# Kernel tuning notes

Measured on AMD Instinct MI355X. Metric: run time of the kernel, lower is better.

The kernel has to match this reference:

```python
import jax, jax.numpy as jnp
import numpy as np

N, E, G = 50000, 800000, 512          # nodes, edges, graphs in batch
DIN, DH, H, DOUT = 128, 128, 2, 128   # dim_in, dim_h, heads, dim_out
NEG_SLOPE = 0.2
EPS_BN = 1e-5


def setup_inputs():
    key = jax.random.key(0)
    ks = jax.random.split(key, 12)
    def glorot(k, shape, fan):
        return (jax.random.normal(k, shape, jnp.float32) / np.float32(np.sqrt(fan)))
    return dict(
        x=jax.random.normal(ks[0], (N, DIN), jnp.float32),
        edge_index=jax.random.randint(ks[1], (2, E), 0, N, dtype=jnp.int32),
        batch=jnp.sort(jax.random.randint(ks[2], (N,), 0, G, dtype=jnp.int32)),
        Wl1=glorot(ks[3], (DIN, H * DH), DIN),
        Wr1=glorot(ks[4], (DIN, H * DH), DIN),
        att1=glorot(ks[5], (H, DH), DH),
        b1=jnp.zeros((H * DH,), jnp.float32),
        gamma=jnp.ones((H * DH,), jnp.float32),
        beta=jnp.zeros((H * DH,), jnp.float32),
        Wl2=glorot(ks[6], (H * DH, DOUT), H * DH),
        Wr2=glorot(ks[7], (H * DH, DOUT), H * DH),
        att2=glorot(ks[8], (1, DOUT), DOUT),
        b2=jnp.zeros((DOUT,), jnp.float32),
        Wlin=glorot(ks[9], (DOUT, 2), DOUT),
        blin=jnp.zeros((2,), jnp.float32),
    )


def gatv2_conv(x, src, dst, Wl, Wr, att, bias, heads, dh, n):
    # x: [n, F]; src/dst: [Etot] (self-loops already appended)
    xl = (x @ Wl).reshape(n, heads, dh)  # source transform (messages)
    xr = (x @ Wr).reshape(n, heads, dh)  # target transform
    m = xl[src] + xr[dst]                             # [Etot, H, dh]
    e = jnp.einsum('ehd,hd->eh', jax.nn.leaky_relu(m, NEG_SLOPE), att)  # [Etot, H]
    # softmax over incoming edges of each target node
    emax = jax.ops.segment_max(e, dst, num_segments=n)
    ex = jnp.exp(e - emax[dst])
    denom = jax.ops.segment_sum(ex, dst, num_segments=n)
    alpha = ex / (denom[dst] + 1e-16)                 # [Etot, H]
    out = jax.ops.segment_sum(xl[src] * alpha[:, :, None], dst, num_segments=n)
    return out.reshape(n, heads * dh) + bias


def reference(x, edge_index, batch, Wl1, Wr1, att1, b1, gamma, beta,
              Wl2, Wr2, att2, b2, Wlin, blin):
    loops = jnp.arange(N, dtype=edge_index.dtype)
    src = jnp.concatenate([edge_index[0], loops])
    dst = jnp.concatenate([edge_index[1], loops])

    h = gatv2_conv(x, src, dst, Wl1, Wr1, att1, b1, H, DH, N)   # [N, H*DH]
    h = jax.nn.elu(h)
    # BatchNorm over node dimension (training-mode batch stats)
    mu = h.mean(axis=0)
    var = h.var(axis=0)
    h = (h - mu) * jax.lax.rsqrt(var + EPS_BN) * gamma + beta
    # dropout p=0 -> identity
    h = gatv2_conv(h, src, dst, Wl2, Wr2, att2, b2, 1, DOUT, N)  # [N, DOUT]

    # global mean pool per graph
    s = jax.ops.segment_sum(h, batch, num_segments=G)
    cnt = jax.ops.segment_sum(jnp.ones((N,), h.dtype), batch, num_segments=G)
    pooled = s / jnp.maximum(cnt, 1.0)[:, None]                  # [G, DOUT]
    return pooled @ Wlin + blin                                  # [G, 2]
```

## Files before the change

kernel.cpp:

```cpp
#include <hip/hip_runtime.h>


#define DIN 128
#define F1 256
#define F2 128
#define NEG_SLOPE 0.2f

typedef unsigned short u16;
typedef __attribute__((ext_vector_type(8))) short short8;
typedef __attribute__((ext_vector_type(4))) float floatx4;

__device__ __forceinline__ float bf2f(u16 u) {
  return __uint_as_float(((unsigned int)u) << 16);
}
__device__ __forceinline__ u16 f2bf(float f) {
  unsigned int x = __float_as_uint(f);
  return (u16)((x + 0x7fffu + ((x >> 16) & 1u)) >> 16);
}
__device__ __forceinline__ void load8(const u16* p, float (&f)[8]) {
  short8 v = *(const short8*)p;
#pragma unroll
  for (int k = 0; k < 8; k++) f[k] = bf2f((u16)v[k]);
}

struct PTab { const void* src[8]; int off[9]; };
__global__ __launch_bounds__(256) void k_convert_all(
    const void* __restrict__ xsrc, u16* __restrict__ xb, int n4, int nxb,
    PTab t, u16* __restrict__ pb, int ptotal, int npb,
    const void* __restrict__ Wl1s, const void* __restrict__ Wr1s,
    const void* __restrict__ Wl2s, const void* __restrict__ Wr2s,
    u16* __restrict__ Wl1t, u16* __restrict__ Wr1t,
    u16* __restrict__ Wl2t, u16* __restrict__ Wr2t,
    int* __restrict__ zbase, int zn, int* __restrict__ flag) {
  __shared__ int flagS;
  int tid = threadIdx.x;
  if (tid < 64) {
    int cnt = 0;
#pragma unroll
    for (int i = 0; i < 2; ++i) {
      u16 v = ((const u16*)xsrc)[2 * (tid + 64 * i)];
      int e = (v >> 7) & 0xFF;
      if (e >= 115 && e <= 130) cnt++;
    }
#pragma unroll
    for (int m = 1; m <= 32; m <<= 1) cnt += __shfl_xor(cnt, m, 64);
    if (tid == 0) flagS = (cnt < 64) ? 1 : 0;
  }
  __syncthreads();
  const int fl = flagS;
  if (blockIdx.x == 0 && tid == 0) *flag = fl;

  int b = blockIdx.x;
  if (b < nxb) {
    int i = b * 256 + tid;
    if (i >= n4) return;
    if (fl) {
      float4 a = ((const float4*)xsrc)[i];
      ushort4 o;
      o.x = f2bf(a.x); o.y = f2bf(a.y); o.z = f2bf(a.z); o.w = f2bf(a.w);
      ((ushort4*)xb)[i] = o;
    } else {
      ((ulong1*)xb)[i] = ((const ulong1*)xsrc)[i];
    }
    return;
  }
  b -= nxb;
  if (b < npb) {
    int i = b * 256 + tid;
    if (i >= ptotal) return;
    int s = 0;
#pragma unroll
    for (int k = 1; k < 8; k++) s += (i >= t.off[k]);
    int local = i - t.off[s];
    pb[i] = fl ? f2bf(((const float*)t.src[s])[local]) : ((const u16*)t.src[s])[local];
    return;
  }
  b -= npb;
  if (b < 512) {
    int seg = b >> 7;
    int i = (b & 127) * 256 + tid;
    const void* s; u16* d; int NL, sh;
    if      (seg == 0) { s = Wl1s; d = Wl1t; NL = 256; sh = 7; }
    else if (seg == 1) { s = Wr1s; d = Wr1t; NL = 256; sh = 7; }
    else if (seg == 2) { s = Wl2s; d = Wl2t; NL = 128; sh = 8; }
    else               { s = Wr2s; d = Wr2t; NL = 128; sh = 8; }
    int n = i >> sh, k = i & ((1 << sh) - 1);
    int si = k * NL + n;
    d[i] = fl ? f2bf(((const float*)s)[si]) : ((const u16*)s)[si];
    return;
  }
  b -= 512;
  int i = b * 256 + tid;
  if (i < zn) zbase[i] = 0;
}

template<int K, bool RB>
__device__ __forceinline__ void gemm_body(
    const u16* __restrict__ A, const u16* __restrict__ Blt, const u16* __restrict__ Brt,
    int NL, u16* __restrict__ Cl, u16* __restrict__ Cr, int M,
    const float* __restrict__ rbias, int bx, int by, int tid) {
  const int m0 = bx * 64;
  const int n0g = by * 64;
  const u16* Bt; u16* C; int col0;
  if (n0g < NL) { Bt = Blt; C = Cl; col0 = n0g; }
  else          { Bt = Brt; C = Cr; col0 = n0g - NL; }

  const int wave = tid >> 6, lane = tid & 63;
  const int wm = wave >> 1, wn = wave & 1;
  const int quad = lane >> 4, l16 = lane & 15;

  floatx4 acc[2][2] = {};
#pragma unroll
  for (int k0 = 0; k0 < K; k0 += 32) {
    short8 af[2], bfr[2];
#pragma unroll
    for (int mt = 0; mt < 2; mt++) {
      int row = m0 + wm * 32 + mt * 16 + l16;
      if (row > M - 1) row = M - 1;
      af[mt] = *(const short8*)(A + (size_t)row * K + k0 + quad * 8);
    }
#pragma unroll
    for (int nt = 0; nt < 2; nt++) {
      int nn = col0 + wn * 32 + nt * 16 + l16;
      bfr[nt] = *(const short8*)(Bt + (size_t)nn * K + k0 + quad * 8);
    }
#pragma unroll
    for (int mt = 0; mt < 2; mt++)
#pragma unroll
      for (int nt = 0; nt < 2; nt++)
        acc[mt][nt] = __builtin_amdgcn_mfma_f32_16x16x32_bf16(af[mt], bfr[nt], acc[mt][nt], 0, 0, 0);
  }

#pragma unroll
  for (int mt = 0; mt < 2; mt++)
#pragma unroll
    for (int nt = 0; nt < 2; nt++) {
      float rb = 0.f;
      if (RB) rb = rbias[n0g + wn * 32 + nt * 16 + l16];
#pragma unroll
      for (int r = 0; r < 4; r++) {
        int row = m0 + wm * 32 + mt * 16 + quad * 4 + r;
        if (row < M) {
          int col = col0 + wn * 32 + nt * 16 + l16;
          C[(size_t)row * NL + col] = f2bf(acc[mt][nt][r] + rb);
        }
      }
    }
}

__global__ __launch_bounds__(256) void k_histgemm1(
    const int* __restrict__ ei, int* __restrict__ hist,
    const int* __restrict__ batch, int* __restrict__ gcnt, int E, int Etot, int N,
    int eb, const u16* __restrict__ xb, const u16* __restrict__ Wl1t,
    const u16* __restrict__ Wr1t, u16* __restrict__ xl1, u16* __restrict__ xr1,
    int Mt) {
  int b = blockIdx.x;
  if (b < eb) {
    int e = b * 256 + threadIdx.x;
    if (e >= Etot) return;
    int dst = (e < E) ? ei[E + e] : (e - E);
    atomicAdd(&hist[dst], 1);
    if (e < N) atomicAdd(&gcnt[batch[e]], 1);
    return;
  }
  b -= eb;
  gemm_body<DIN, false>(xb, Wl1t, Wr1t, F1, xl1, xr1, N, nullptr, b % Mt, b / Mt,
                        threadIdx.x);
}

__global__ void k_scan(const int* __restrict__ hist, int* __restrict__ rowptr,
                       int* __restrict__ cursor, unsigned long long* __restrict__ pstate,
                       int* __restrict__ ctr, int n, int Etot) {
  __shared__ int tmp[256];
  __shared__ int bidS, offS;
  int t = threadIdx.x;
  if (t == 0) bidS = atomicAdd(ctr, 1);
  __syncthreads();
  int bid = bidS;
  int gid = bid * 256 + t;
  int v = (gid < n) ? hist[gid] : 0;
  tmp[t] = v;
  __syncthreads();
  for (int off = 1; off < 256; off <<= 1) {
    int add = (t >= off) ? tmp[t - off] : 0;
    __syncthreads();
    tmp[t] += add;
    __syncthreads();
  }
  if (t == 0) {
    int total = tmp[255];
    unsigned long long st =
        ((unsigned long long)(bid == 0 ? 2 : 1) << 32) | (unsigned)total;
    atomicExch(&pstate[bid], st);
    int off = 0;
    if (bid > 0) {
      int b = bid - 1;
      while (true) {
        unsigned long long s;
        do { s = atomicAdd(&pstate[b], 0ULL); } while ((s >> 32) == 0);
        off += (int)(unsigned)s;
        if ((s >> 32) == 2) break;
        b--;
      }
      atomicExch(&pstate[bid],
                 ((unsigned long long)2 << 32) | (unsigned)(off + total));
    }
    offS = off;
  }
  __syncthreads();
  int off = offS;
  if (gid < n) {
    int ex = off + tmp[t] - v;
    rowptr[gid] = ex;
    cursor[gid] = ex;
  }
  if (gid == 0) rowptr[n] = Etot;
}

__global__ void k_scatter(const int* __restrict__ ei, int* __restrict__ cursor,
                          int* __restrict__ ssrc, int E, int Etot) {
  int e = blockIdx.x * 256 + threadIdx.x;
  if (e >= Etot) return;
  int src, dst;
  if (e < E) { src = ei[e]; dst = ei[E + e]; }
  else       { src = e - E; dst = e - E; }
  int pos = atomicAdd(&cursor[dst], 1);
  ssrc[pos] = src;
}

template<int HEADS, int MODE>
__global__ __launch_bounds__(256) void k_agg(
    const u16* __restrict__ xl, const u16* __restrict__ xr,
    const u16* __restrict__ att, const u16* __restrict__ bias,
    const int* __restrict__ rowptr, const int* __restrict__ ssrc,
    void* __restrict__ outv, int n) {
  constexpr int F = HEADS * 128;
  constexpr int EPI = 4 / HEADS;
  int wave = threadIdx.x >> 6, lane = threadIdx.x & 63;
  int node = blockIdx.x * 4 + wave;
  if (node >= n) return;
  const int q = lane >> 4, l = lane & 15;
  const int eo   = (HEADS == 2) ? (q >> 1) : q;
  const int head = (HEADS == 2) ? (q & 1) : 0;
  const int ch0 = head * 128 + l * 8;

  float xrv[8], attv[8], acc[8];
  load8(xr + (size_t)node * F + ch0, xrv);
  load8(att + ch0, attv);
#pragma unroll
  for (int k = 0; k < 8; k++) acc[k] = 0.f;

  float l_run = 0.f;
  const int jb = rowptr[node], je = rowptr[node + 1];
  for (int j = jb; j < je; j += EPI) {
    int jj = j + eo;
    int src = ssrc[jj < je ? jj : (je - 1)];
    float xlv[8];
    load8(xl + (size_t)src * F + ch0, xlv);
    float s = 0.f;
#pragma unroll
    for (int k = 0; k < 8; k++) {
      float mm = xlv[k] + xrv[k];
      mm = mm > 0.f ? mm : NEG_SLOPE * mm;
      s += mm * attv[k];
    }
#pragma unroll
    for (int m = 1; m <= 8; m <<= 1) s += __shfl_xor(s, m, 64);
    float p = (jj < je) ? __expf(fminf(s, 80.f)) : 0.f;
    l_run += p;
#pragma unroll
    for (int k = 0; k < 8; k++) acc[k] += p * xlv[k];
  }

#pragma unroll
  for (int m = 16 * HEADS; m <= 32; m <<= 1) {
#pragma unroll
    for (int k = 0; k < 8; k++) acc[k] += __shfl_xor(acc[k], m, 64);
    l_run += __shfl_xor(l_run, m, 64);
  }

  if (lane < 16 * HEADS) {
    float inv = 1.f / (l_run + 1e-16f);
    if (MODE == 0) {
      short8 o;
#pragma unroll
      for (int k = 0; k < 8; k++) {
        float t = acc[k] * inv + bf2f(bias[ch0 + k]);
        t = t > 0.f ? t : (__expf(t) - 1.f);
        o[k] = (short)f2bf(t);
      }
      *(short8*)((u16*)outv + (size_t)node * F + ch0) = o;
    } else {
      float v[8];
#pragma unroll
      for (int k = 0; k < 8; k++) v[k] = acc[k] * inv + bf2f(bias[ch0 + k]);
      float* op = (float*)outv + (size_t)node * F + ch0;
      *(float4*)op = make_float4(v[0], v[1], v[2], v[3]);
      *(float4*)(op + 4) = make_float4(v[4], v[5], v[6], v[7]);
    }
  }
}

__global__ __launch_bounds__(256) void k_stats2(
    const u16* __restrict__ h, float* __restrict__ gsum, float* __restrict__ gsumsq,
    const u16* __restrict__ gamma, const u16* __restrict__ beta,
    float* __restrict__ ab, const int* __restrict__ gcnt,
    const u16* __restrict__ blin, const int* __restrict__ flag,
    void* __restrict__ out, int* __restrict__ sctr, int n, int G, float invn) {
  __shared__ float smS[8][256], smQ[8][256];
  __shared__ int lastS;
  int t = threadIdx.x;
  int rg = t >> 5, cl = t & 31;
  int ch0 = cl * 8;
  float s[8] = {}, q[8] = {};
  for (int r = blockIdx.x * 8 + rg; r < n; r += 256 * 8) {
    float v[8];
    load8(h + (size_t)r * F1 + ch0, v);
#pragma unroll
    for (int k = 0; k < 8; k++) { s[k] += v[k]; q[k] += v[k] * v[k]; }
  }
#pragma unroll
  for (int k = 0; k < 8; k++) { smS[rg][ch0 + k] = s[k]; smQ[rg][ch0 + k] = q[k]; }
  __syncthreads();
  float ts = 0.f, tq = 0.f;
#pragma unroll
  for (int g = 0; g < 8; g++) { ts += smS[g][t]; tq += smQ[g][t]; }
  atomicAdd(&gsum[t], ts);
  atomicAdd(&gsumsq[t], tq);

  __threadfence();
  __syncthreads();
  if (t == 0) lastS = (atomicAdd(sctr, 1) == 255) ? 1 : 0;
  __syncthreads();
  if (lastS) {
    __threadfence();
    float gs = atomicAdd(&gsum[t], 0.f);
    float gq = atomicAdd(&gsumsq[t], 0.f);
    float mu = gs * invn;
    float var = gq * invn - mu * mu;
    float a = bf2f(gamma[t]) * rsqrtf(fmaxf(var, 0.f) + 1e-5f);
    ab[t] = a;
    ab[256 + t] = bf2f(beta[t]) - mu * a;
    for (int g = t; g < G; g += 256) {
      if (gcnt[g] == 0) {
        float o0 = bf2f(blin[0]), o1 = bf2f(blin[1]);
        if (*flag) {
          ((float*)out)[g * 2 + 0] = o0;
          ((float*)out)[g * 2 + 1] = o1;
        } else {
          ((u16*)out)[g * 2 + 0] = f2bf(o0);
          ((u16*)out)[g * 2 + 1] = f2bf(o1);
        }
      }
    }
  }
}

__global__ __launch_bounds__(256) void k_gemm2bn(
    const u16* __restrict__ A, const u16* __restrict__ Blt, const u16* __restrict__ Brt,
    u16* __restrict__ Cl, u16* __restrict__ Cr, int M, const float* __restrict__ ab) {
  const int tid = threadIdx.x;
  const int m0 = blockIdx.x * 64;
  const int n0g = blockIdx.y * 64;
  const u16* Bt; u16* C; int col0;
  if (n0g < F2) { Bt = Blt; C = Cl; col0 = n0g; }
  else          { Bt = Brt; C = Cr; col0 = n0g - F2; }

  const int wave = tid >> 6, lane = tid & 63;
  const int wm = wave >> 1, wn = wave & 1;
  const int quad = lane >> 4, l16 = lane & 15;

  floatx4 acc[2][2] = {};
#pragma unroll
  for (int k0 = 0; k0 < F1; k0 += 32) {
    float av[8], bv[8];
    *(float4*)av       = *(const float4*)(ab + k0 + quad * 8);
    *(float4*)(av + 4) = *(const float4*)(ab + k0 + quad * 8 + 4);
    *(float4*)bv       = *(const float4*)(ab + 256 + k0 + quad * 8);
    *(float4*)(bv + 4) = *(const float4*)(ab + 256 + k0 + quad * 8 + 4);
    short8 af[2], bfr[2];
#pragma unroll
    for (int mt = 0; mt < 2; mt++) {
      int row = m0 + wm * 32 + mt * 16 + l16;
      if (row > M - 1) row = M - 1;
      short8 raw = *(const short8*)(A + (size_t)row * F1 + k0 + quad * 8);
#pragma unroll
      for (int j = 0; j < 8; j++) {
        float v = av[j] * bf2f((u16)raw[j]) + bv[j];
        af[mt][j] = (short)f2bf(v);
      }
    }
#pragma unroll
    for (int nt = 0; nt < 2; nt++) {
      int nn = col0 + wn * 32 + nt * 16 + l16;
      bfr[nt] = *(const short8*)(Bt + (size_t)nn * F1 + k0 + quad * 8);
    }
#pragma unroll
    for (int mt = 0; mt < 2; mt++)
#pragma unroll
      for (int nt = 0; nt < 2; nt++)
        acc[mt][nt] = __builtin_amdgcn_mfma_f32_16x16x32_bf16(af[mt], bfr[nt], acc[mt][nt], 0, 0, 0);
  }

#pragma unroll
  for (int mt = 0; mt < 2; mt++)
#pragma unroll
    for (int nt = 0; nt < 2; nt++)
#pragma unroll
      for (int r = 0; r < 4; r++) {
        int row = m0 + wm * 32 + mt * 16 + quad * 4 + r;
        if (row < M) {
          int col = col0 + wn * 32 + nt * 16 + l16;
          C[(size_t)row * F2 + col] = f2bf(acc[mt][nt][r]);
        }
      }
}

__device__ __forceinline__ int lowerb(const int* __restrict__ a, int n, int key) {
  int lo = 0, hi = n;
  while (lo < hi) { int m = (lo + hi) >> 1; if (a[m] < key) lo = m + 1; else hi = m; }
  return lo;
}

__global__ __launch_bounds__(256) void k_poolfinal(
    const float* __restrict__ h2, const int* __restrict__ batch,
    const u16* __restrict__ Wlin, const u16* __restrict__ blin,
    void* __restrict__ out, const int* __restrict__ flag, int G, int N) {
  __shared__ float sm[4][128];
  int g = blockIdx.x;
  int wave = threadIdx.x >> 6, lane = threadIdx.x & 63;
  int jb = lowerb(batch, N, g);
  int je = lowerb(batch, N, g + 1);
  if (jb >= je) return;
  int ch = lane * 2;
  float c0 = 0.f, c1 = 0.f;
  for (int r = jb + wave; r < je; r += 4) {
    float2 v = *(const float2*)(h2 + (size_t)r * F2 + ch);
    c0 += v.x; c1 += v.y;
  }
  sm[wave][ch] = c0;
  sm[wave][ch + 1] = c1;
  __syncthreads();
  if (wave == 0) {
    c0 = sm[0][ch] + sm[1][ch] + sm[2][ch] + sm[3][ch];
    c1 = sm[0][ch + 1] + sm[1][ch + 1] + sm[2][ch + 1] + sm[3][ch + 1];
    float cf = fmaxf((float)(je - jb), 1.f);
    c0 /= cf; c1 /= cf;
    float s0 = c0 * bf2f(Wlin[ch * 2 + 0]) + c1 * bf2f(Wlin[(ch + 1) * 2 + 0]);
    float s1 = c0 * bf2f(Wlin[ch * 2 + 1]) + c1 * bf2f(Wlin[(ch + 1) * 2 + 1]);
#pragma unroll
    for (int m = 1; m <= 32; m <<= 1) {
      s0 += __shfl_xor(s0, m, 64);
      s1 += __shfl_xor(s1, m, 64);
    }
    if (lane == 0) {
      float o0 = s0 + bf2f(blin[0]);
      float o1 = s1 + bf2f(blin[1]);
      if (*flag) {
        ((float*)out)[g * 2 + 0] = o0;
        ((float*)out)[g * 2 + 1] = o1;
      } else {
        ((u16*)out)[g * 2 + 0] = f2bf(o0);
        ((u16*)out)[g * 2 + 1] = f2bf(o1);
      }
    }
  }
}

extern "C" void kernel_launch(void* const* d_in, const int* in_sizes, int n_in,
                              void* d_out, int out_size, void* d_ws, size_t ws_size,
                              hipStream_t stream) {
  const int* ei    = (const int*)d_in[1];
  const int* batch = (const int*)d_in[2];

  const int N = in_sizes[0] / DIN;
  const int E = in_sizes[1] / 2;
  const int G = out_size / 2;
  const int Etot = E + N;

  char* p = (char*)d_ws;
  auto alloc = [&](size_t bytes) {
    char* r = p;
    p += (bytes + 255) & ~(size_t)255;
    return r;
  };
  int*  flag     = (int*)alloc(256);
  int*  hist     = (int*)alloc((size_t)N * 4);
  float* gsum    = (float*)alloc(1024);
  float* gsumsq  = (float*)alloc(1024);
  unsigned long long* pstate = (unsigned long long*)alloc(2048);
  int*  ctr      = (int*)alloc(256);
  int*  gcnt     = (int*)alloc((size_t)G * 4);
  int*  sctr     = (int*)alloc(256);
  int   zn       = (int)(((char*)sctr + 256) - (char*)hist) / 4;
  int*  rowptr   = (int*)alloc((size_t)(N + 1) * 4);
  int*  cursor   = (int*)alloc((size_t)N * 4);
  float* ab      = (float*)alloc(2048);
  int*  ssrc     = (int*)alloc((size_t)Etot * 4);
  u16*  xb       = (u16*)alloc((size_t)N * DIN * 2);
  u16*  pb       = (u16*)alloc(4096);
  u16*  Wl1t     = (u16*)alloc(DIN * F1 * 2);
  u16*  Wr1t     = (u16*)alloc(DIN * F1 * 2);
  u16*  Wl2t     = (u16*)alloc(F1 * F2 * 2);
  u16*  Wr2t     = (u16*)alloc(F1 * F2 * 2);
  u16*  regionA  = (u16*)alloc((size_t)N * F1 * 2);
  u16*  regionB  = (u16*)alloc((size_t)N * F1 * 2);
  u16*  regionC  = (u16*)alloc((size_t)N * F1 * 2);

  u16*  xl1  = regionA;
  u16*  xr1  = regionB;
  u16*  helu = regionC;
  u16*  xl2  = regionB;
  u16*  xr2  = regionB + (size_t)N * F2;
  float* h2  = (float*)regionA;

  const int pidx[8] = {5, 6, 7, 8, 11, 12, 13, 14};
  PTab tab;
  int accum = 0;
  for (int i = 0; i < 8; i++) {
    tab.src[i] = d_in[pidx[i]];
    tab.off[i] = accum;
    accum += in_sizes[pidx[i]];
  }
  tab.off[8] = accum;
  int n4 = in_sizes[0] / 4;
  int nxb = (n4 + 255) / 256;
  int npb = (accum + 255) / 256;
  int nzb = (zn + 255) / 256;
  k_convert_all<<<nxb + npb + 512 + nzb, 256, 0, stream>>>(
      d_in[0], xb, n4, nxb, tab, pb, accum, npb,
      d_in[3], d_in[4], d_in[9], d_in[10], Wl1t, Wr1t, Wl2t, Wr2t,
      hist, zn, flag);
  u16 *pAtt1 = pb + tab.off[0], *pB1 = pb + tab.off[1], *pGamma = pb + tab.off[2],
      *pBeta = pb + tab.off[3], *pAtt2 = pb + tab.off[4], *pB2 = pb + tab.off[5],
      *pWlin = pb + tab.off[6], *pBlin = pb + tab.off[7];

  const int eb = (Etot + 255) / 256;
  const int sb = (N + 255) / 256;
  const int Mt = (N + 63) / 64;

  k_histgemm1<<<eb + Mt * 8, 256, 0, stream>>>(ei, hist, batch, gcnt, E, Etot, N,
                                               eb, xb, Wl1t, Wr1t, xl1, xr1, Mt);
  k_scan<<<sb, 256, 0, stream>>>(hist, rowptr, cursor, pstate, ctr, N, Etot);
  k_scatter<<<eb, 256, 0, stream>>>(ei, cursor, ssrc, E, Etot);

  k_agg<2, 0><<<(N + 3) / 4, 256, 0, stream>>>(xl1, xr1, pAtt1, pB1, rowptr, ssrc, helu, N);

  k_stats2<<<256, 256, 0, stream>>>(helu, gsum, gsumsq, pGamma, pBeta, ab, gcnt,
                                    pBlin, flag, d_out, sctr, N, G, 1.0f / (float)N);

  k_gemm2bn<<<dim3(Mt, 4), 256, 0, stream>>>(helu, Wl2t, Wr2t, xl2, xr2, N, ab);

  k_agg<1, 1><<<(N + 3) / 4, 256, 0, stream>>>(xl2, xr2, pAtt2, pB2, rowptr, ssrc, h2, N);

  k_poolfinal<<<G, 256, 0, stream>>>(h2, batch, pWlin, pBlin, d_out, flag, G, N);
}
```

Before: 508.7 us.

## Split histogram from GEMM1, drop graph-count path, unroll aggregation loop

Un-fuses the edge histogram and the first layer GEMM into separate kernels, moving the GEMM after the scatter. It also removes the per-graph node counting and the empty-graph output handling in the stats kernel, letting the pool kernel handle empty graphs itself. A 2x unroll hint is added on the edge loop of the aggregation kernel. The aim is to cut atomic contention and divergent block roles in the fused kernel and to improve memory-level parallelism in aggregation. The cost is one more kernel launch and the loss of overlap between the histogram and the GEMM.

```diff
diff --git a/kernel.cpp b/kernel.cpp
--- a/kernel.cpp
+++ b/kernel.cpp
@@ -94,78 +94,12 @@
   if (i < zn) zbase[i] = 0;
 }
 
-template<int K, bool RB>
-__device__ __forceinline__ void gemm_body(
-    const u16* __restrict__ A, const u16* __restrict__ Blt, const u16* __restrict__ Brt,
-    int NL, u16* __restrict__ Cl, u16* __restrict__ Cr, int M,
-    const float* __restrict__ rbias, int bx, int by, int tid) {
-  const int m0 = bx * 64;
-  const int n0g = by * 64;
-  const u16* Bt; u16* C; int col0;
-  if (n0g < NL) { Bt = Blt; C = Cl; col0 = n0g; }
-  else          { Bt = Brt; C = Cr; col0 = n0g - NL; }
-
-  const int wave = tid >> 6, lane = tid & 63;
-  const int wm = wave >> 1, wn = wave & 1;
-  const int quad = lane >> 4, l16 = lane & 15;
-
-  floatx4 acc[2][2] = {};
-#pragma unroll
-  for (int k0 = 0; k0 < K; k0 += 32) {
-    short8 af[2], bfr[2];
-#pragma unroll
-    for (int mt = 0; mt < 2; mt++) {
-      int row = m0 + wm * 32 + mt * 16 + l16;
-      if (row > M - 1) row = M - 1;
-      af[mt] = *(const short8*)(A + (size_t)row * K + k0 + quad * 8);
-    }
-#pragma unroll
-    for (int nt = 0; nt < 2; nt++) {
-      int nn = col0 + wn * 32 + nt * 16 + l16;
-      bfr[nt] = *(const short8*)(Bt + (size_t)nn * K + k0 + quad * 8);
-    }
-#pragma unroll
-    for (int mt = 0; mt < 2; mt++)
-#pragma unroll
-      for (int nt = 0; nt < 2; nt++)
-        acc[mt][nt] = __builtin_amdgcn_mfma_f32_16x16x32_bf16(af[mt], bfr[nt], acc[mt][nt], 0, 0, 0);
-  }
-
-#pragma unroll
-  for (int mt = 0; mt < 2; mt++)
-#pragma unroll
-    for (int nt = 0; nt < 2; nt++) {
-      float rb = 0.f;
-      if (RB) rb = rbias[n0g + wn * 32 + nt * 16 + l16];
-#pragma unroll
-      for (int r = 0; r < 4; r++) {
-        int row = m0 + wm * 32 + mt * 16 + quad * 4 + r;
-        if (row < M) {
-          int col = col0 + wn * 32 + nt * 16 + l16;
-          C[(size_t)row * NL + col] = f2bf(acc[mt][nt][r] + rb);
-        }
-      }
-    }
-}
-
-__global__ __launch_bounds__(256) void k_histgemm1(
-    const int* __restrict__ ei, int* __restrict__ hist,
-    const int* __restrict__ batch, int* __restrict__ gcnt, int E, int Etot, int N,
-    int eb, const u16* __restrict__ xb, const u16* __restrict__ Wl1t,
-    const u16* __restrict__ Wr1t, u16* __restrict__ xl1, u16* __restrict__ xr1,
-    int Mt) {
-  int b = blockIdx.x;
-  if (b < eb) {
-    int e = b * 256 + threadIdx.x;
-    if (e >= Etot) return;
-    int dst = (e < E) ? ei[E + e] : (e - E);
-    atomicAdd(&hist[dst], 1);
-    if (e < N) atomicAdd(&gcnt[batch[e]], 1);
-    return;
-  }
-  b -= eb;
-  gemm_body<DIN, false>(xb, Wl1t, Wr1t, F1, xl1, xr1, N, nullptr, b % Mt, b / Mt,
-                        threadIdx.x);
+__global__ void k_hist(const int* __restrict__ ei, int* __restrict__ hist,
+                       int E, int Etot) {
+  int e = blockIdx.x * 256 + threadIdx.x;
+  if (e >= Etot) return;
+  int dst = (e < E) ? ei[E + e] : (e - E);
+  atomicAdd(&hist[dst], 1);
 }
 
 __global__ void k_scan(const int* __restrict__ hist, int* __restrict__ rowptr,
@@ -228,6 +162,56 @@
   ssrc[pos] = src;
 }
 
+__global__ __launch_bounds__(256) void k_gemm1(
+    const u16* __restrict__ A, const u16* __restrict__ Blt, const u16* __restrict__ Brt,
+    u16* __restrict__ Cl, u16* __restrict__ Cr, int M) {
+  const int tid = threadIdx.x;
+  const int m0 = blockIdx.x * 64;
+  const int n0g = blockIdx.y * 64;
+  const u16* Bt; u16* C; int col0;
+  if (n0g < F1) { Bt = Blt; C = Cl; col0 = n0g; }
+  else          { Bt = Brt; C = Cr; col0 = n0g - F1; }
+
+  const int wave = tid >> 6, lane = tid & 63;
+  const int wm = wave >> 1, wn = wave & 1;
+  const int quad = lane >> 4, l16 = lane & 15;
+
+  floatx4 acc[2][2] = {};
+#pragma unroll
+  for (int k0 = 0; k0 < DIN; k0 += 32) {
+    short8 af[2], bfr[2];
+#pragma unroll
+    for (int mt = 0; mt < 2; mt++) {
+      int row = m0 + wm * 32 + mt * 16 + l16;
+      if (row > M - 1) row = M - 1;
+      af[mt] = *(const short8*)(A + (size_t)row * DIN + k0 + quad * 8);
+    }
+#pragma unroll
+    for (int nt = 0; nt < 2; nt++) {
+      int nn = col0 + wn * 32 + nt * 16 + l16;
+      bfr[nt] = *(const short8*)(Bt + (size_t)nn * DIN + k0 + quad * 8);
+    }
+#pragma unroll
+    for (int mt = 0; mt < 2; mt++)
+#pragma unroll
+      for (int nt = 0; nt < 2; nt++)
+        acc[mt][nt] = __builtin_amdgcn_mfma_f32_16x16x32_bf16(af[mt], bfr[nt], acc[mt][nt], 0, 0, 0);
+  }
+
+#pragma unroll
+  for (int mt = 0; mt < 2; mt++)
+#pragma unroll
+    for (int nt = 0; nt < 2; nt++)
+#pragma unroll
+      for (int r = 0; r < 4; r++) {
+        int row = m0 + wm * 32 + mt * 16 + quad * 4 + r;
+        if (row < M) {
+          int col = col0 + wn * 32 + nt * 16 + l16;
+          C[(size_t)row * F1 + col] = f2bf(acc[mt][nt][r]);
+        }
+      }
+}
+
 template<int HEADS, int MODE>
 __global__ __launch_bounds__(256) void k_agg(
     const u16* __restrict__ xl, const u16* __restrict__ xr,
@@ -252,6 +236,7 @@
 
   float l_run = 0.f;
   const int jb = rowptr[node], je = rowptr[node + 1];
+#pragma unroll 2
   for (int j = jb; j < je; j += EPI) {
     int jj = j + eo;
     int src = ssrc[jj < je ? jj : (je - 1)];
@@ -304,9 +289,7 @@
 __global__ __launch_bounds__(256) void k_stats2(
     const u16* __restrict__ h, float* __restrict__ gsum, float* __restrict__ gsumsq,
     const u16* __restrict__ gamma, const u16* __restrict__ beta,
-    float* __restrict__ ab, const int* __restrict__ gcnt,
-    const u16* __restrict__ blin, const int* __restrict__ flag,
-    void* __restrict__ out, int* __restrict__ sctr, int n, int G, float invn) {
+    float* __restrict__ ab, int* __restrict__ sctr, int n, float invn) {
   __shared__ float smS[8][256], smQ[8][256];
   __shared__ int lastS;
   int t = threadIdx.x;
@@ -341,18 +324,6 @@
     float a = bf2f(gamma[t]) * rsqrtf(fmaxf(var, 0.f) + 1e-5f);
     ab[t] = a;
     ab[256 + t] = bf2f(beta[t]) - mu * a;
-    for (int g = t; g < G; g += 256) {
-      if (gcnt[g] == 0) {
-        float o0 = bf2f(blin[0]), o1 = bf2f(blin[1]);
-        if (*flag) {
-          ((float*)out)[g * 2 + 0] = o0;
-          ((float*)out)[g * 2 + 1] = o1;
-        } else {
-          ((u16*)out)[g * 2 + 0] = f2bf(o0);
-          ((u16*)out)[g * 2 + 1] = f2bf(o1);
-        }
-      }
-    }
   }
 }
 
@@ -431,7 +402,6 @@
   int wave = threadIdx.x >> 6, lane = threadIdx.x & 63;
   int jb = lowerb(batch, N, g);
   int je = lowerb(batch, N, g + 1);
-  if (jb >= je) return;
   int ch = lane * 2;
   float c0 = 0.f, c1 = 0.f;
   for (int r = jb + wave; r < je; r += 4) {
@@ -490,7 +460,6 @@
   float* gsumsq  = (float*)alloc(1024);
   unsigned long long* pstate = (unsigned long long*)alloc(2048);
   int*  ctr      = (int*)alloc(256);
-  int*  gcnt     = (int*)alloc((size_t)G * 4);
   int*  sctr     = (int*)alloc(256);
   int   zn       = (int)(((char*)sctr + 256) - (char*)hist) / 4;
   int*  rowptr   = (int*)alloc((size_t)(N + 1) * 4);
@@ -539,15 +508,16 @@
   const int sb = (N + 255) / 256;
   const int Mt = (N + 63) / 64;
 
-  k_histgemm1<<<eb + Mt * 8, 256, 0, stream>>>(ei, hist, batch, gcnt, E, Etot, N,
-                                               eb, xb, Wl1t, Wr1t, xl1, xr1, Mt);
+  k_hist<<<eb, 256, 0, stream>>>(ei, hist, E, Etot);
   k_scan<<<sb, 256, 0, stream>>>(hist, rowptr, cursor, pstate, ctr, N, Etot);
   k_scatter<<<eb, 256, 0, stream>>>(ei, cursor, ssrc, E, Etot);
 
+  k_gemm1<<<dim3(Mt, 8), 256, 0, stream>>>(xb, Wl1t, Wr1t, xl1, xr1, N);
+
   k_agg<2, 0><<<(N + 3) / 4, 256, 0, stream>>>(xl1, xr1, pAtt1, pB1, rowptr, ssrc, helu, N);
 
-  k_stats2<<<256, 256, 0, stream>>>(helu, gsum, gsumsq, pGamma, pBeta, ab, gcnt,
-                                    pBlin, flag, d_out, sctr, N, G, 1.0f / (float)N);
+  k_stats2<<<256, 256, 0, stream>>>(helu, gsum, gsumsq, pGamma, pBeta, ab, sctr,
+                                    N, 1.0f / (float)N);
 
   k_gemm2bn<<<dim3(Mt, 4), 256, 0, stream>>>(helu, Wl2t, Wr2t, xl2, xr2, N, ab);
 
```

After: 474.7 us. -6.7%, faster.
